# Performance work log

Hardware: AMD Instinct MI355X
Metric: run time of the kernel (lower is better)

The kernel has to match this reference:

```python
import jax, jax.numpy as jnp
import numpy as np

POS = np.array([[0,3,0.5],[0,3,1.5],[0,3,2.5],[0,3,3.5],[0,3,4.5],[0,3,5.5],[1,0,0],[1,6,6],[2,0,6],[2,6,0],[3,0,0],[3,6,6],[4,0,6],[4,6,0],[5,0,0],[5,6,6],[6,0,6],[6,6,0],[7,0,0],[7,6,6],[8,0,6],[8,6,0],[9,0,0],[9,6,6],[10,0,6],[10,6,0],[11,0,0],[11,6,6],[12,0,6],[12,6,0],[13,0,0],[13,6,6],[14,0,6],[14,6,0],[15,0,0],[15,6,6],[16,0,6],[16,6,0],[17,0.5,0.5],[17,3,0.5],[17,5.5,0.5],[17,0.5,3],[17,3,3],[17,5.5,3],[17,0.5,5.5],[17,3,5.5],[17,5.5,5.5]], dtype=np.float32)  # (47,3) fixed buffer

B, S, D, H, FF, HID = 512, 47, 32, 4, 2048, 256

def _ln(x, w, b, eps=1e-5):
    mu = jnp.mean(x, -1, keepdims=True)
    var = jnp.mean((x - mu) ** 2, -1, keepdims=True)
    return (x - mu) * jax.lax.rsqrt(var + eps) * w + b

def _encoder_layer(h, wi, bi, wo, bo, l1w, l1b, f1w, f1b, f2w, f2b, l2w, l2b):
    # torch post-norm TransformerEncoderLayer; batch_first=False => attention over axis 0
    L, N, E = h.shape
    Dh = E // H
    qkv = h @ wi.T + bi                                  # (L,N,3E)
    q, k, v = jnp.split(qkv, 3, axis=-1)
    q = q.reshape(L, N, H, Dh); k = k.reshape(L, N, H, Dh); v = v.reshape(L, N, H, Dh)
    scores = jnp.einsum('lnhd,mnhd->nhlm', q, k) * (1.0 / np.sqrt(Dh))  # (N,H,L,L)
    a = jax.nn.softmax(scores, axis=-1)
    o = jnp.einsum('nhlm,mnhd->lnhd', a, v).reshape(L, N, E)
    h = _ln(h + (o @ wo.T + bo), l1w, l1b)
    ff = jax.nn.relu(h @ f1w.T + f1b) @ f2w.T + f2b
    return _ln(h + ff, l2w, l2b)

def setup_inputs():
    key = jax.random.key(0)
    ks = list(jax.random.split(key, 24))
    rn = lambda k, s, sc=0.05: jax.random.normal(k, s, jnp.float32) * sc
    return dict(
        x=jax.random.normal(ks[0], (B, S), jnp.float32),
        w_in=rn(ks[1], (D, 1)), b_in=rn(ks[2], (D,)),
        w_pos=rn(ks[3], (D, 3)), b_pos=rn(ks[4], (D,)),
        cls_token=rn(ks[5], (1, 1, D), 1.0),
        attn_in_w=rn(ks[6], (2, 3 * D, D)), attn_in_b=rn(ks[7], (2, 3 * D)),
        attn_out_w=rn(ks[8], (2, D, D)), attn_out_b=rn(ks[9], (2, D)),
        ln1_w=jnp.ones((2, D)), ln1_b=jnp.zeros((2, D)),
        ff1_w=rn(ks[10], (2, FF, D)), ff1_b=rn(ks[11], (2, FF)),
        ff2_w=rn(ks[12], (2, D, FF)), ff2_b=rn(ks[13], (2, D)),
        ln2_w=jnp.ones((2, D)), ln2_b=jnp.zeros((2, D)),
        out_w=rn(ks[14], (1, D)), out_b=rn(ks[15], (1,)),
        mlp_w0=rn(ks[16], (HID, S)), mlp_b0=rn(ks[17], (HID,)),
        mlp_w1=rn(ks[18], (HID, HID)), mlp_b1=rn(ks[19], (HID,)),
        mlp_w2=rn(ks[20], (1, HID)), mlp_b2=rn(ks[21], (1,)),
    )

def reference(x, w_in, b_in, w_pos, b_pos, cls_token, attn_in_w, attn_in_b, attn_out_w, attn_out_b, ln1_w, ln1_b, ff1_w, ff1_b, ff2_w, ff2_b, ln2_w, ln2_b, out_w, out_b, mlp_w0, mlp_b0, mlp_w1, mlp_b1, mlp_w2, mlp_b2):
    Bn = x.shape[0]
    h = x[..., None] * w_in[:, 0] + b_in                 # Linear(1,D): (B,S,D)
    h = h + (jnp.asarray(POS) @ w_pos.T + b_pos)         # pos projection (S,D)
    cls = jnp.broadcast_to(cls_token, (Bn, 1, D))
    h = jnp.concatenate([cls, h], axis=1)                # (B,S+1,D)
    for i in range(2):
        h = _encoder_layer(h, attn_in_w[i], attn_in_b[i], attn_out_w[i], attn_out_b[i], ln1_w[i], ln1_b[i], ff1_w[i], ff1_b[i], ff2_w[i], ff2_b[i], ln2_w[i], ln2_b[i])
    out = jax.nn.relu(h[:, 1:, :] @ out_w.T + out_b)[..., 0]   # (B,S); dropout = eval identity
    o = jax.nn.relu(out @ mlp_w0.T + mlp_b0)
    o = jax.nn.relu(o @ mlp_w1.T + mlp_b1)
    o = jax.nn.relu(o @ mlp_w2.T + mlp_b2)               # MLP ends with ReLU per source
    return o
```

## Files before the change

### kernel.cpp

```cpp
#include <hip/hip_runtime.h>

#define NB 512
#define NS 47
#define NP 48
#define DIM 32
#define NFF 2048
#define NHID 256
#define NROWS (NB * NP)
#define FTOK 96

#define VSTR 520
#define PSTR 72

typedef _Float16 f16x8 __attribute__((ext_vector_type(8)));
typedef _Float16 f16x4 __attribute__((ext_vector_type(4)));
typedef float f32x4 __attribute__((ext_vector_type(4)));

__constant__ float POSC[NS * 3] = {
  0,3,0.5f, 0,3,1.5f, 0,3,2.5f, 0,3,3.5f, 0,3,4.5f, 0,3,5.5f,
  1,0,0, 1,6,6, 2,0,6, 2,6,0, 3,0,0, 3,6,6, 4,0,6, 4,6,0,
  5,0,0, 5,6,6, 6,0,6, 6,6,0, 7,0,0, 7,6,6, 8,0,6, 8,6,0,
  9,0,0, 9,6,6, 10,0,6, 10,6,0, 11,0,0, 11,6,6, 12,0,6, 12,6,0,
  13,0,0, 13,6,6, 14,0,6, 14,6,0, 15,0,0, 15,6,6, 16,0,6, 16,6,0,
  17,0.5f,0.5f, 17,3,0.5f, 17,5.5f,0.5f, 17,0.5f,3, 17,3,3, 17,5.5f,3,
  17,0.5f,5.5f, 17,3,5.5f, 17,5.5f,5.5f
};

__global__ __launch_bounds__(256) void prep_embed_kernel(
    const float* __restrict__ w1, const float* __restrict__ w2,
    _Float16* __restrict__ w1h, _Float16* __restrict__ w2h,
    const float* __restrict__ x, const float* __restrict__ w_in,
    const float* __restrict__ b_in, const float* __restrict__ w_pos,
    const float* __restrict__ b_pos, const float* __restrict__ cls,
    float* __restrict__ h) {
  const int bx = blockIdx.x;
  if (bx < 512) {
    int idx = bx * 256 + threadIdx.x;
    w1h[idx] = (_Float16)w1[idx];
    int l = idx >> 16, r = idx & 65535, d = r >> 11, ff = r & 2047;
    int dst = ((l * 64 + (ff >> 5)) * 32 + d) * 32 + (ff & 31);
    w2h[dst] = (_Float16)w2[idx];
    return;
  }
  int idx = (bx - 512) * 256 + threadIdx.x;
  int r = idx >> 5, d = idx & 31;
  int l = r / NP, n = r - l * NP;
  float v;
  if (n == 0) {
    v = cls[d];
  } else {
    int s = n - 1;
    v = x[l * NS + s] * w_in[d] + b_in[d]
      + POSC[s * 3 + 0] * w_pos[d * 3 + 0]
      + POSC[s * 3 + 1] * w_pos[d * 3 + 1]
      + POSC[s * 3 + 2] * w_pos[d * 3 + 2] + b_pos[d];
  }
  h[idx] = v;
}

__global__ __launch_bounds__(256) void kv_kernel(
    const float* __restrict__ h, const float* __restrict__ wi, const float* __restrict__ bi,
    _Float16* __restrict__ Kp, _Float16* __restrict__ Vt) {
  __shared__ float ws_[512];
  __shared__ float bs_[16];
  const int t = threadIdx.x;
  const int nh = blockIdx.x >> 1;
  const int n = nh >> 2, hh = nh & 3;
  const int l = ((blockIdx.x & 1) << 8) | t;
  for (int i = t; i < 512; i += 256) {
    int sub = i >> 8, rem = i & 255;
    int jj = rem >> 5, d = rem & 31;
    ws_[i] = wi[((sub + 1) * 32 + hh * 8 + jj) * 32 + d];
  }
  if (t < 16) bs_[t] = bi[((t >> 3) + 1) * 32 + hh * 8 + (t & 7)];
  __syncthreads();
  const float4* hrow = (const float4*)(h + (l * NP + n) * 32);
  float4 hv[8];
  #pragma unroll
  for (int i = 0; i < 8; ++i) hv[i] = hrow[i];
  f16x8 kh, kl_, vh;
  #pragma unroll
  for (int jj = 0; jj < 8; ++jj) {
    float k0 = bs_[jj], k1 = 0.f, k2 = 0.f, k3 = 0.f;
    float v0 = bs_[8 + jj], v1 = 0.f, v2 = 0.f, v3 = 0.f;
    #pragma unroll
    for (int d4 = 0; d4 < 8; ++d4) {
      float4 hvv = hv[d4];
      k0 += hvv.x * ws_[jj * 32 + 4 * d4 + 0];
      k1 += hvv.y * ws_[jj * 32 + 4 * d4 + 1];
      k2 += hvv.z * ws_[jj * 32 + 4 * d4 + 2];
      k3 += hvv.w * ws_[jj * 32 + 4 * d4 + 3];
      v0 += hvv.x * ws_[256 + jj * 32 + 4 * d4 + 0];
      v1 += hvv.y * ws_[256 + jj * 32 + 4 * d4 + 1];
      v2 += hvv.z * ws_[256 + jj * 32 + 4 * d4 + 2];
      v3 += hvv.w * ws_[256 + jj * 32 + 4 * d4 + 3];
    }
    float kv = (k0 + k1) + (k2 + k3);
    float vv = (v0 + v1) + (v2 + v3);
    kh[jj] = (_Float16)kv; kl_[jj] = (_Float16)(kv - (float)kh[jj]);
    vh[jj] = (_Float16)vv;
  }
  _Float16* kdst = Kp + ((size_t)nh * 512 + l) * 16;
  *(f16x8*)(kdst) = kh;
  *(f16x8*)(kdst + 8) = kl_;
  #pragma unroll
  for (int d = 0; d < 8; ++d) Vt[(size_t)nh * 4096 + d * 512 + l] = vh[d];
}

__global__ __launch_bounds__(256, 3) void attn_mfma_kernel(
    const float* __restrict__ h, const float* __restrict__ wi, const float* __restrict__ bi,
    const _Float16* __restrict__ Kp, const _Float16* __restrict__ Vt,
    float* __restrict__ o) {
  __shared__ alignas(16) _Float16 khi[512 * 8];
  __shared__ alignas(16) _Float16 klo[512 * 8];
  __shared__ alignas(16) _Float16 vts[8 * VSTR];
  __shared__ alignas(16) float hq_pls[4608];
  __shared__ alignas(16) _Float16 qf[128 * 16];
  __shared__ float wsq[256];
  __shared__ float bq[8];
  const int bx = blockIdx.x;
  const int nh = bx >> 2, qc = bx & 3;
  const int n = nh >> 2, hh = nh & 3;
  const int t = threadIdx.x;
  const int lane = t & 63, wv = t >> 6;
  const int c = lane & 15, g = lane >> 4;

  const _Float16* kg = Kp + (size_t)nh * 8192;
  for (int r = t; r < 512; r += 256) {
    const uint4* src = (const uint4*)(kg + r * 16);
    uint4 a = src[0], b = src[1];
    *(uint4*)(khi + r * 8) = a;
    *(uint4*)(klo + r * 8) = b;
  }
  {
    const _Float16* vg = Vt + (size_t)nh * 4096;
    for (int i = t; i < 512; i += 256) {
      int d = i >> 6, seg = i & 63;
      *(uint4*)(vts + d * VSTR + seg * 8) = *(const uint4*)(vg + d * 512 + seg * 8);
    }
  }
  wsq[t] = wi[(hh * 8 + (t & 7)) * 32 + (t >> 3)];
  if (t < 8) bq[t] = bi[hh * 8 + t];
  float* hq = hq_pls;

  #pragma unroll
  for (int rp = 0; rp < 2; ++rp) {
    {
      int row = t >> 2, quar = t & 3;
      const float4* src =
          (const float4*)(h + (((qc * 128 + rp * 64 + row) * NP) + n) * 32 + quar * 8);
      float4 a = src[0], b = src[1];
      __syncthreads();
      *(float4*)(hq + row * 36 + quar * 8) = a;
      *(float4*)(hq + row * 36 + quar * 8 + 4) = b;
    }
    __syncthreads();
    {
      int row = t >> 2, pr = t & 3;
      #pragma unroll
      for (int u = 0; u < 2; ++u) {
        int jj = pr * 2 + u;
        float a = bq[jj];
        #pragma unroll
        for (int d = 0; d < 32; ++d) a += hq[row * 36 + d] * wsq[d * 8 + jj];
        _Float16 qh = (_Float16)a;
        _Float16 ql = (_Float16)(a - (float)qh);
        qf[(rp * 64 + row) * 16 + jj] = qh;
        qf[(rp * 64 + row) * 16 + 8 + jj] = ql;
      }
    }
    __syncthreads();
  }

  const f16x8 hz = {(_Float16)0,(_Float16)0,(_Float16)0,(_Float16)0,
                    (_Float16)0,(_Float16)0,(_Float16)0,(_Float16)0};
  const f32x4 zf = {0.f, 0.f, 0.f, 0.f};
  _Float16* pls_ = (_Float16*)hq_pls;
  _Float16* mypA = pls_ + wv * (16 * PSTR);
  _Float16* mypB = pls_ + (4 + wv) * (16 * PSTR);
  const int q0A = qc * 128 + wv * 16;
  const int q0B = q0A + 64;

  f16x8 aqA = hz, aqB = hz;
  if (g < 3) {
    aqA = *(const f16x8*)(qf + (wv * 16 + c) * 16 + (g & 1) * 8);
    aqB = *(const f16x8*)(qf + (64 + wv * 16 + c) * 16 + (g & 1) * 8);
  }
  f32x4 accA = {0.f, 0.f, 0.f, 0.f}, accB = {0.f, 0.f, 0.f, 0.f};
  float lsA[4] = {0.f, 0.f, 0.f, 0.f}, lsB[4] = {0.f, 0.f, 0.f, 0.f};

  for (int ch = 0; ch < 8; ++ch) {
    const int kb = ch * 64;
    #pragma unroll
    for (int kt = 0; kt < 4; ++kt) {
      f16x8 bk = hz;
      if (g < 2)       bk = *(const f16x8*)(khi + (kb + kt * 16 + c) * 8);
      else if (g == 2) bk = *(const f16x8*)(klo + (kb + kt * 16 + c) * 8);
      f32x4 sA = __builtin_amdgcn_mfma_f32_16x16x32_f16(aqA, bk, zf, 0, 0, 0);
      f32x4 sB = __builtin_amdgcn_mfma_f32_16x16x32_f16(aqB, bk, zf, 0, 0, 0);
      #pragma unroll
      for (int r = 0; r < 4; ++r) {
        float pA = __expf(sA[r] * 0.35355339059327373f - 2.0f);
        float pB = __expf(sB[r] * 0.35355339059327373f - 2.0f);
        _Float16 phA = (_Float16)pA;
        _Float16 phB = (_Float16)pB;
        lsA[r] += (float)phA;
        lsB[r] += (float)phB;
        mypA[(g * 4 + r) * PSTR + kt * 16 + c] = phA;
        mypB[(g * 4 + r) * PSTR + kt * 16 + c] = phB;
      }
    }
    #pragma unroll
    for (int half = 0; half < 2; ++half) {
      f16x8 bv = hz;
      if (c < 8) bv = *(const f16x8*)(vts + c * VSTR + kb + half * 32 + g * 8);
      f16x8 apA = *(const f16x8*)(mypA + c * PSTR + half * 32 + g * 8);
      f16x8 apB = *(const f16x8*)(mypB + c * PSTR + half * 32 + g * 8);
      accA = __builtin_amdgcn_mfma_f32_16x16x32_f16(apA, bv, accA, 0, 0, 0);
      accB = __builtin_amdgcn_mfma_f32_16x16x32_f16(apB, bv, accB, 0, 0, 0);
    }
  }
  #pragma unroll
  for (int m = 1; m < 16; m <<= 1) {
    #pragma unroll
    for (int r = 0; r < 4; ++r) {
      lsA[r] += __shfl_xor(lsA[r], m, 64);
      lsB[r] += __shfl_xor(lsB[r], m, 64);
    }
  }
  if (c < 8) {
    #pragma unroll
    for (int r = 0; r < 4; ++r) {
      o[((q0A + g * 4 + r) * NP + n) * 32 + hh * 8 + c] = accA[r] / lsA[r];
      o[((q0B + g * 4 + r) * NP + n) * 32 + hh * 8 + c] = accB[r] / lsB[r];
    }
  }
}

__global__ __launch_bounds__(256) void proj_ln1_kernel(
    const float* __restrict__ o, const float* __restrict__ wo, const float* __restrict__ bo,
    const float* __restrict__ lw, const float* __restrict__ lb, float* __restrict__ h) {
  __shared__ float wos[32 * 33];
  __shared__ float pre[64 * 33];
  const int g = blockIdx.x, t = threadIdx.x;
  for (int i = t; i < 1024; i += 256) wos[(i >> 5) * 33 + (i & 31)] = wo[i];
  __syncthreads();
  const int subr = t >> 2, jq = t & 3;
  const int r = g * 64 + subr;
  const float4* orow = (const float4*)(o + r * 32);
  float4 ov[8];
  #pragma unroll
  for (int i = 0; i < 8; ++i) ov[i] = orow[i];
  const float* hres = h + r * 32 + jq * 8;
  #pragma unroll
  for (int jj = 0; jj < 8; ++jj) {
    int j = jq * 8 + jj;
    float a0 = bo[j], a1 = 0.f, a2 = 0.f, a3 = 0.f;
    #pragma unroll
    for (int d4 = 0; d4 < 8; ++d4) {
      float4 vv = ov[d4];
      a0 += vv.x * wos[j * 33 + 4 * d4 + 0];
      a1 += vv.y * wos[j * 33 + 4 * d4 + 1];
      a2 += vv.z * wos[j * 33 + 4 * d4 + 2];
      a3 += vv.w * wos[j * 33 + 4 * d4 + 3];
    }
    pre[subr * 33 + j] = (a0 + a1) + (a2 + a3) + hres[jj];
  }
  __syncthreads();
  if (t < 64) {
    float mu = 0.f;
    #pragma unroll
    for (int d = 0; d < 32; ++d) mu += pre[t * 33 + d];
    mu *= (1.f / 32.f);
    float var = 0.f;
    #pragma unroll
    for (int d = 0; d < 32; ++d) { float dv = pre[t * 33 + d] - mu; var += dv * dv; }
    float rs = rsqrtf(var * (1.f / 32.f) + 1e-5f);
    float* hrow = h + (g * 64 + t) * 32;
    #pragma unroll
    for (int d = 0; d < 32; ++d)
      hrow[d] = (pre[t * 33 + d] - mu) * rs * lw[d] + lb[d];
  }
}

__global__ __launch_bounds__(256, 1) void ff_fused_kernel(
    const float* __restrict__ h, const _Float16* __restrict__ w1h,
    const float* __restrict__ b1, const _Float16* __restrict__ w2h,
    const float* __restrict__ b2, const float* __restrict__ lw,
    const float* __restrict__ lb, const float* __restrict__ ow,
    const float* __restrict__ ob,
    const float* __restrict__ m0w, const float* __restrict__ m0b,
    const float* __restrict__ m1w, const float* __restrict__ m1b,
    const float* __restrict__ m2w, const float* __restrict__ m2b,
    float* __restrict__ out, int do_head) {
  __shared__ alignas(16) float yw[4][FTOK * 33];
  __shared__ alignas(16) float pre_s[FTOK * 33];
  __shared__ float sv2[2][48];
  __shared__ float hid[NHID];
  __shared__ float red[4];
  const int t = threadIdx.x;
  const int lane = t & 63;
  const int wv = t >> 6;
  const int nl = lane & 15;
  const int g = lane >> 4;
  const int g4 = g * 4;
  const int r0 = blockIdx.x * FTOK;

  f16x8 hfrag[6];
  #pragma unroll
  for (int tt = 0; tt < 6; ++tt) {
    const float4 h0 = *(const float4*)(h + (r0 + tt * 16 + nl) * 32 + g * 8);
    const float4 h1 = *(const float4*)(h + (r0 + tt * 16 + nl) * 32 + g * 8 + 4);
    hfrag[tt][0] = (_Float16)h0.x; hfrag[tt][1] = (_Float16)h0.y;
    hfrag[tt][2] = (_Float16)h0.z; hfrag[tt][3] = (_Float16)h0.w;
    hfrag[tt][4] = (_Float16)h1.x; hfrag[tt][5] = (_Float16)h1.y;
    hfrag[tt][6] = (_Float16)h1.z; hfrag[tt][7] = (_Float16)h1.w;
  }

  f32x4 acc0[6], acc1[6];
  #pragma unroll
  for (int tt = 0; tt < 6; ++tt) {
    acc0[tt] = (f32x4){0.f, 0.f, 0.f, 0.f};
    acc1[tt] = (f32x4){0.f, 0.f, 0.f, 0.f};
  }
  const f32x4 zero = {0.f, 0.f, 0.f, 0.f};

  for (int sc = 0; sc < 16; ++sc) {
    const int ffb = wv * 512 + sc * 32;
    f16x8 wf0 = *(const f16x8*)(w1h + (ffb + nl) * 32 + g * 8);
    f16x8 wf1 = *(const f16x8*)(w1h + (ffb + 16 + nl) * 32 + g * 8);
    float4 bv0 = *(const float4*)(b1 + ffb + g4);
    float4 bv1 = *(const float4*)(b1 + ffb + 16 + g4);
    const _Float16* cb = w2h + (ffb >> 5) * 1024;
    f16x4 a0lo = *(const f16x4*)(cb + nl * 32 + g4);
    f16x4 a0hi = *(const f16x4*)(cb + nl * 32 + 16 + g4);
    f16x4 a1lo = *(const f16x4*)(cb + (16 + nl) * 32 + g4);
    f16x4 a1hi = *(const f16x4*)(cb + (16 + nl) * 32 + 16 + g4);
    f16x8 A0, A1;
    #pragma unroll
    for (int j = 0; j < 4; ++j) {
      A0[j] = a0lo[j]; A0[4 + j] = a0hi[j];
      A1[j] = a1lo[j]; A1[4 + j] = a1hi[j];
    }
    #pragma unroll
    for (int tt = 0; tt < 6; ++tt) {
      f32x4 cc0 = __builtin_amdgcn_mfma_f32_16x16x32_f16(wf0, hfrag[tt], zero, 0, 0, 0);
      f32x4 cc1 = __builtin_amdgcn_mfma_f32_16x16x32_f16(wf1, hfrag[tt], zero, 0, 0, 0);
      f16x8 uB;
      uB[0] = (_Float16)fmaxf(cc0[0] + bv0.x, 0.f);
      uB[1] = (_Float16)fmaxf(cc0[1] + bv0.y, 0.f);
      uB[2] = (_Float16)fmaxf(cc0[2] + bv0.z, 0.f);
      uB[3] = (_Float16)fmaxf(cc0[3] + bv0.w, 0.f);
      uB[4] = (_Float16)fmaxf(cc1[0] + bv1.x, 0.f);
      uB[5] = (_Float16)fmaxf(cc1[1] + bv1.y, 0.f);
      uB[6] = (_Float16)fmaxf(cc1[2] + bv1.z, 0.f);
      uB[7] = (_Float16)fmaxf(cc1[3] + bv1.w, 0.f);
      acc0[tt] = __builtin_amdgcn_mfma_f32_16x16x32_f16(A0, uB, acc0[tt], 0, 0, 0);
      acc1[tt] = __builtin_amdgcn_mfma_f32_16x16x32_f16(A1, uB, acc1[tt], 0, 0, 0);
    }
  }
  #pragma unroll
  for (int tt = 0; tt < 6; ++tt) {
    #pragma unroll
    for (int r = 0; r < 4; ++r) {
      yw[wv][(tt * 16 + nl) * 33 + g4 + r]      = acc0[tt][r];
      yw[wv][(tt * 16 + nl) * 33 + 16 + g4 + r] = acc1[tt][r];
    }
  }
  __syncthreads();

  {
    int idx = t;
    #pragma unroll
    for (int u = 0; u < 12; ++u, idx += 256) {
      int tok = idx >> 5, d = idx & 31;
      int off = tok * 33 + d;
      float v = yw[0][off] + yw[1][off] + yw[2][off] + yw[3][off]
              + b2[d] + h[(r0 + tok) * 32 + d];
      pre_s[off] = v;
    }
  }
  __syncthreads();

  if (t < FTOK) {
    float mu = 0.f;
    #pragma unroll
    for (int d = 0; d < 32; ++d) mu += pre_s[t * 33 + d];
    mu *= (1.f / 32.f);
    float var = 0.f;
    #pragma unroll
    for (int d = 0; d < 32; ++d) { float dv = pre_s[t * 33 + d] - mu; var += dv * dv; }
    float rs = rsqrtf(var * (1.f / 32.f) + 1e-5f);
    const int rr = r0 + t;
    float* hrow = (float*)h + (size_t)rr * 32;
    float hn[32];
    #pragma unroll
    for (int d = 0; d < 32; ++d) {
      hn[d] = (pre_s[t * 33 + d] - mu) * rs * lw[d] + lb[d];
      hrow[d] = hn[d];
    }
    if (do_head) {
      int ll = t / 48, n = t - ll * 48;
      if (n > 0) {
        float a = ob[0];
        #pragma unroll
        for (int d = 0; d < 32; ++d) a += hn[d] * ow[d];
        sv2[ll][n - 1] = fmaxf(a, 0.f);
      }
    }
  }

  if (do_head) {
    __syncthreads();
    for (int ll = 0; ll < 2; ++ll) {
      const int l = (r0 / 48) + ll;
      {
        float a = m0b[t];
        const float* wr = m0w + t * NS;
        #pragma unroll
        for (int s = 0; s < NS; ++s) a += sv2[ll][s] * wr[s];
        hid[t] = fmaxf(a, 0.f);
      }
      __syncthreads();
      {
        float a = m1b[t];
        const float4* wr = (const float4*)(m1w + t * NHID);
        #pragma unroll 8
        for (int j4 = 0; j4 < 64; ++j4) {
          float4 w = wr[j4];
          a += hid[4 * j4 + 0] * w.x + hid[4 * j4 + 1] * w.y
             + hid[4 * j4 + 2] * w.z + hid[4 * j4 + 3] * w.w;
        }
        float h2 = fmaxf(a, 0.f);
        float part = h2 * m2w[t];
        #pragma unroll
        for (int off = 32; off > 0; off >>= 1) part += __shfl_down(part, off, 64);
        if ((t & 63) == 0) red[t >> 6] = part;
      }
      __syncthreads();
      if (t == 0) out[l] = fmaxf(red[0] + red[1] + red[2] + red[3] + m2b[0], 0.f);
      __syncthreads();
    }
  }
}

extern "C" void kernel_launch(void* const* d_in, const int* in_sizes, int n_in,
                              void* d_out, int out_size, void* d_ws, size_t ws_size,
                              hipStream_t stream) {
  (void)in_sizes; (void)n_in; (void)out_size; (void)ws_size;
  const float* x     = (const float*)d_in[0];
  const float* w_in  = (const float*)d_in[1];
  const float* b_in  = (const float*)d_in[2];
  const float* w_pos = (const float*)d_in[3];
  const float* b_pos = (const float*)d_in[4];
  const float* cls   = (const float*)d_in[5];
  const float* wi    = (const float*)d_in[6];
  const float* bi    = (const float*)d_in[7];
  const float* wo    = (const float*)d_in[8];
  const float* bo    = (const float*)d_in[9];
  const float* l1w   = (const float*)d_in[10];
  const float* l1b   = (const float*)d_in[11];
  const float* f1w   = (const float*)d_in[12];
  const float* f1b   = (const float*)d_in[13];
  const float* f2w   = (const float*)d_in[14];
  const float* f2b   = (const float*)d_in[15];
  const float* l2w   = (const float*)d_in[16];
  const float* l2b   = (const float*)d_in[17];
  const float* ow    = (const float*)d_in[18];
  const float* ob    = (const float*)d_in[19];
  const float* m0w   = (const float*)d_in[20];
  const float* m0b   = (const float*)d_in[21];
  const float* m1w   = (const float*)d_in[22];
  const float* m1b   = (const float*)d_in[23];
  const float* m2w   = (const float*)d_in[24];
  const float* m2b   = (const float*)d_in[25];
  float* out = (float*)d_out;

  float* ws   = (float*)d_ws;
  float* h    = ws;
  float* o    = ws + 786432;
  float* R2   = ws + 1572864;
  _Float16* Kp = (_Float16*)R2;
  _Float16* Vt = (_Float16*)(R2 + 786432);
  _Float16* w1h = (_Float16*)(ws + 2776576);
  _Float16* w2h = (_Float16*)(ws + 2842112);

  prep_embed_kernel<<<3584, 256, 0, stream>>>(f1w, f2w, w1h, w2h,
                                              x, w_in, b_in, w_pos, b_pos, cls, h);
  for (int L = 0; L < 2; ++L) {
    kv_kernel<<<384, 256, 0, stream>>>(h, wi + L * 3072, bi + L * 96, Kp, Vt);
    attn_mfma_kernel<<<768, 256, 0, stream>>>(h, wi + L * 3072, bi + L * 96, Kp, Vt, o);
    proj_ln1_kernel<<<384, 256, 0, stream>>>(o, wo + L * 1024, bo + L * 32,
                                             l1w + L * 32, l1b + L * 32, h);
    ff_fused_kernel<<<256, 256, 0, stream>>>(h, w1h + L * 65536, f1b + L * NFF,
                                             w2h + L * 65536, f2b + L * 32,
                                             l2w + L * 32, l2b + L * 32,
                                             ow, ob, m0w, m0b, m1w, m1b, m2w, m2b,
                                             out, L);
  }
}
```

Baseline: 151.2 us.

## Stage FF weights through double-buffered LDS with register prefetch and pre-swizzled W2

The fused FF kernel now stages each 32-wide chunk of W1 and the W2 fragment into a double-buffered LDS region. The next chunk is prefetched into registers while the current chunk's MFMAs run, and the b1 bias is loaded into LDS once. The W2 prep permutation is changed so each lane reads its A-fragment as one contiguous 16-byte load, with no gather from two f16x4 pieces. The cost is two block-wide barriers per chunk plus larger shared memory aliased with the reduction buffers, and the min-blocks launch bound is dropped.

```diff
diff --git a/kernel.cpp b/kernel.cpp
--- a/kernel.cpp
+++ b/kernel.cpp
@@ -38,7 +38,11 @@
     int idx = bx * 256 + threadIdx.x;
     w1h[idx] = (_Float16)w1[idx];
     int l = idx >> 16, r = idx & 65535, d = r >> 11, ff = r & 2047;
-    int dst = ((l * 64 + (ff >> 5)) * 32 + d) * 32 + (ff & 31);
+    int c = ff >> 5, ffl = ff & 31;
+    int tab = d >> 4, nl = d & 15;
+    int hi = ffl >> 4, g = (ffl & 15) >> 2, j = (ffl & 3) + hi * 4;
+    int lam = g * 16 + nl;
+    int dst = (l * 64 + c) * 1024 + tab * 512 + lam * 8 + j;
     w2h[dst] = (_Float16)w2[idx];
     return;
   }
@@ -283,7 +287,7 @@
   }
 }
 
-__global__ __launch_bounds__(256, 1) void ff_fused_kernel(
+__global__ __launch_bounds__(256) void ff_fused_kernel(
     const float* __restrict__ h, const _Float16* __restrict__ w1h,
     const float* __restrict__ b1, const _Float16* __restrict__ w2h,
     const float* __restrict__ b2, const float* __restrict__ lw,
@@ -293,11 +297,16 @@
     const float* __restrict__ m1w, const float* __restrict__ m1b,
     const float* __restrict__ m2w, const float* __restrict__ m2b,
     float* __restrict__ out, int do_head) {
-  __shared__ alignas(16) float yw[4][FTOK * 33];
-  __shared__ alignas(16) float pre_s[FTOK * 33];
+  __shared__ alignas(16) char smem[63360];
   __shared__ float sv2[2][48];
   __shared__ float hid[NHID];
   __shared__ float red[4];
+  _Float16* wbuf = (_Float16*)smem;
+  float* bias_lds = (float*)(smem + 32768);
+  float* yw = (float*)smem;
+  float* pre_s = (float*)(smem + 50688 * 4 / 4 * 4);
+  pre_s = (float*)(smem + 4 * FTOK * 33 * 4);
+
   const int t = threadIdx.x;
   const int lane = t & 63;
   const int wv = t >> 6;
@@ -317,6 +326,34 @@
     hfrag[tt][6] = (_Float16)h1.z; hfrag[tt][7] = (_Float16)h1.w;
   }
 
+  {
+    const _Float16* g1 = w1h + (wv * 512) * 32;
+    const _Float16* g2 = w2h + (wv * 16) * 1024;
+    uint4 a = *(const uint4*)(g1 + lane * 8);
+    uint4 b = *(const uint4*)(g1 + 512 + lane * 8);
+    uint4 c = *(const uint4*)(g2 + lane * 8);
+    uint4 d = *(const uint4*)(g2 + 512 + lane * 8);
+    _Float16* d1 = wbuf + wv * 2048;
+    *(uint4*)(d1 + lane * 8) = a;
+    *(uint4*)(d1 + 512 + lane * 8) = b;
+    *(uint4*)(d1 + 1024 + lane * 8) = c;
+    *(uint4*)(d1 + 1536 + lane * 8) = d;
+    const float4* bsrc = (const float4*)b1;
+    float4 ba = bsrc[t * 2], bb = bsrc[t * 2 + 1];
+    *(float4*)(bias_lds + t * 8) = ba;
+    *(float4*)(bias_lds + t * 8 + 4) = bb;
+  }
+  uint4 sr0, sr1, sr2, sr3;
+  {
+    const _Float16* g1 = w1h + (wv * 512 + 32) * 32;
+    const _Float16* g2 = w2h + (wv * 16 + 1) * 1024;
+    sr0 = *(const uint4*)(g1 + lane * 8);
+    sr1 = *(const uint4*)(g1 + 512 + lane * 8);
+    sr2 = *(const uint4*)(g2 + lane * 8);
+    sr3 = *(const uint4*)(g2 + 512 + lane * 8);
+  }
+  __syncthreads();
+
   f32x4 acc0[6], acc1[6];
   #pragma unroll
   for (int tt = 0; tt < 6; ++tt) {
@@ -326,22 +363,13 @@
   const f32x4 zero = {0.f, 0.f, 0.f, 0.f};
 
   for (int sc = 0; sc < 16; ++sc) {
-    const int ffb = wv * 512 + sc * 32;
-    f16x8 wf0 = *(const f16x8*)(w1h + (ffb + nl) * 32 + g * 8);
-    f16x8 wf1 = *(const f16x8*)(w1h + (ffb + 16 + nl) * 32 + g * 8);
-    float4 bv0 = *(const float4*)(b1 + ffb + g4);
-    float4 bv1 = *(const float4*)(b1 + ffb + 16 + g4);
-    const _Float16* cb = w2h + (ffb >> 5) * 1024;
-    f16x4 a0lo = *(const f16x4*)(cb + nl * 32 + g4);
-    f16x4 a0hi = *(const f16x4*)(cb + nl * 32 + 16 + g4);
-    f16x4 a1lo = *(const f16x4*)(cb + (16 + nl) * 32 + g4);
-    f16x4 a1hi = *(const f16x4*)(cb + (16 + nl) * 32 + 16 + g4);
-    f16x8 A0, A1;
-    #pragma unroll
-    for (int j = 0; j < 4; ++j) {
-      A0[j] = a0lo[j]; A0[4 + j] = a0hi[j];
-      A1[j] = a1lo[j]; A1[4 + j] = a1hi[j];
-    }
+    const _Float16* s1 = wbuf + (sc & 1) * 8192 + wv * 2048;
+    f16x8 wf0 = *(const f16x8*)(s1 + nl * 32 + g * 8);
+    f16x8 wf1 = *(const f16x8*)(s1 + 512 + nl * 32 + g * 8);
+    f16x8 A0  = *(const f16x8*)(s1 + 1024 + lane * 8);
+    f16x8 A1  = *(const f16x8*)(s1 + 1536 + lane * 8);
+    float4 bv0 = *(const float4*)(bias_lds + wv * 512 + sc * 32 + g4);
+    float4 bv1 = *(const float4*)(bias_lds + wv * 512 + sc * 32 + 16 + g4);
     #pragma unroll
     for (int tt = 0; tt < 6; ++tt) {
       f32x4 cc0 = __builtin_amdgcn_mfma_f32_16x16x32_f16(wf0, hfrag[tt], zero, 0, 0, 0);
@@ -358,13 +386,32 @@
       acc0[tt] = __builtin_amdgcn_mfma_f32_16x16x32_f16(A0, uB, acc0[tt], 0, 0, 0);
       acc1[tt] = __builtin_amdgcn_mfma_f32_16x16x32_f16(A1, uB, acc1[tt], 0, 0, 0);
     }
-  }
+    if (sc < 15) {
+      __syncthreads();
+      _Float16* d1 = wbuf + ((sc + 1) & 1) * 8192 + wv * 2048;
+      *(uint4*)(d1 + lane * 8) = sr0;
+      *(uint4*)(d1 + 512 + lane * 8) = sr1;
+      *(uint4*)(d1 + 1024 + lane * 8) = sr2;
+      *(uint4*)(d1 + 1536 + lane * 8) = sr3;
+      if (sc < 14) {
+        const _Float16* g1 = w1h + (wv * 512 + (sc + 2) * 32) * 32;
+        const _Float16* g2 = w2h + (wv * 16 + (sc + 2)) * 1024;
+        sr0 = *(const uint4*)(g1 + lane * 8);
+        sr1 = *(const uint4*)(g1 + 512 + lane * 8);
+        sr2 = *(const uint4*)(g2 + lane * 8);
+        sr3 = *(const uint4*)(g2 + 512 + lane * 8);
+      }
+      __syncthreads();
+    }
+  }
+  __syncthreads();
+
   #pragma unroll
   for (int tt = 0; tt < 6; ++tt) {
     #pragma unroll
     for (int r = 0; r < 4; ++r) {
-      yw[wv][(tt * 16 + nl) * 33 + g4 + r]      = acc0[tt][r];
-      yw[wv][(tt * 16 + nl) * 33 + 16 + g4 + r] = acc1[tt][r];
+      yw[wv * (FTOK * 33) + (tt * 16 + nl) * 33 + g4 + r]      = acc0[tt][r];
+      yw[wv * (FTOK * 33) + (tt * 16 + nl) * 33 + 16 + g4 + r] = acc1[tt][r];
     }
   }
   __syncthreads();
@@ -375,8 +422,8 @@
     for (int u = 0; u < 12; ++u, idx += 256) {
       int tok = idx >> 5, d = idx & 31;
       int off = tok * 33 + d;
-      float v = yw[0][off] + yw[1][off] + yw[2][off] + yw[3][off]
-              + b2[d] + h[(r0 + tok) * 32 + d];
+      float v = yw[off] + yw[FTOK * 33 + off] + yw[2 * FTOK * 33 + off]
+              + yw[3 * FTOK * 33 + off] + b2[d] + h[(r0 + tok) * 32 + d];
       pre_s[off] = v;
     }
   }
```

New measurement: 153.4 us. About the same (+1.4%).
